# Kernel optimization log

Measured on AMD Instinct MI355X. Metric: run time of the kernel, lower is better.

## Reference

```python
import jax, jax.numpy as jnp
import numpy as np

N = 50000
E = 800000
H = 4
C = 64
IN = 61
NEG_SLOPE = 0.2


def setup_inputs() -> dict:
    key = jax.random.key(0)
    ks = jax.random.split(key, 20)
    x = jax.random.normal(ks[0], (N, IN), dtype=jnp.float32)
    edge_index = jax.random.randint(ks[1], (2, E), 0, N, dtype=jnp.int64)

    def glorot(k, shape):
        fan = shape[0] + shape[-1] if len(shape) == 2 else shape[-1] * 2
        s = jnp.sqrt(6.0 / fan)
        return jax.random.uniform(k, shape, jnp.float32, -s, s)

    dims = [IN, H * C, H * C]
    params = {}
    for i, din in enumerate(dims):
        params[f'w{i}'] = glorot(ks[2 + 4 * i], (din, H * C))
        params[f'att_src{i}'] = glorot(ks[3 + 4 * i], (H, C))
        params[f'att_dst{i}'] = glorot(ks[4 + 4 * i], (H, C))
        params[f'b{i}'] = jnp.zeros((H * C,), jnp.float32)
    params['head_w1'] = glorot(ks[14], (H * C, C))
    params['head_b1'] = jnp.zeros((C,), jnp.float32)
    params['head_w2'] = glorot(ks[15], (C, 1))
    params['head_b2'] = jnp.zeros((1,), jnp.float32)
    return dict(x=x, edge_index=edge_index, **params)


def _gat_layer(x, W, att_src, att_dst, bias, src, dst):
    # Linear transform -> [N, H, C]
    h = (x @ W).reshape(N, H, C)
    # Per-node attention logits
    a_src = jnp.einsum('nhc,hc->nh', h, att_src)  # [N, H]
    a_dst = jnp.einsum('nhc,hc->nh', h, att_dst)
    # Per-edge score, leaky relu
    e = jax.nn.leaky_relu(a_src[src] + a_dst[dst], NEG_SLOPE)  # [Etot, H]
    # Segment softmax over incoming edges of each dst node
    m = jax.ops.segment_max(e, dst, num_segments=N)  # [N, H]
    ex = jnp.exp(e - m[dst])
    denom = jax.ops.segment_sum(ex, dst, num_segments=N)
    alpha = ex / denom[dst]  # [Etot, H]
    # Scatter-aggregate messages
    out = jax.ops.segment_sum(h[src] * alpha[:, :, None], dst, num_segments=N)  # [N, H, C]
    return out.reshape(N, H * C) + bias


def reference(x, edge_index, w0, att_src0, att_dst0, b0,
              w1, att_src1, att_dst1, b1,
              w2, att_src2, att_dst2, b2,
              head_w1, head_b1, head_w2, head_b2):
    # PyG GATConv adds self-loops by default
    loop = jnp.arange(N, dtype=edge_index.dtype)
    src = jnp.concatenate([edge_index[0], loop])
    dst = jnp.concatenate([edge_index[1], loop])

    layers = [(w0, att_src0, att_dst0, b0),
              (w1, att_src1, att_dst1, b1),
              (w2, att_src2, att_dst2, b2)]
    h = x
    for (W, a_s, a_d, b) in layers:
        h = _gat_layer(h, W, a_s, a_d, b, src, dst)
        h = jax.nn.elu(h)  # dropout is identity in eval mode
    # MLP head
    h = jax.nn.relu(h @ head_w1 + head_b1)
    out = (h @ head_w2 + head_b2).squeeze(-1)  # [N]
    return out
```

## Files before the change

### kernel.cpp

```cpp
#include <hip/hip_runtime.h>
#include <cstdint>
#include <cstddef>

#define NN   50000
#define EE   800000
#define ETOT (EE + NN)
#define HC   256
#define NEG_SLOPE 0.2f
#define SENT_WORDS 25000
#define SENT_VAL 0x42C80000u

typedef __attribute__((ext_vector_type(8))) short g4_bf16x8;
typedef __attribute__((ext_vector_type(4))) float g4_f32x4;

__device__ __forceinline__ float g4_bf2f(unsigned short h) {
    union { unsigned int u; float f; } v;
    v.u = ((unsigned int)h) << 16;
    return v.f;
}
__device__ __forceinline__ unsigned short g4_f2bf(float f) {
    union { float f; unsigned int u; } v;
    v.f = f;
    unsigned int u = v.u;
    u += 0x7fffu + ((u >> 16) & 1u);
    return (unsigned short)(u >> 16);
}
__device__ __forceinline__ float g4_ld(const void* p, size_t i, int isf) {
    return isf ? ((const float*)p)[i] : g4_bf2f(((const unsigned short*)p)[i]);
}

__global__ void g4_init(const unsigned int* __restrict__ xw,
                        const int* __restrict__ ei32, int* __restrict__ flags,
                        int* __restrict__ deg, int* __restrict__ cnt,
                        unsigned int* __restrict__ outw) {
    if (blockIdx.x == 0) {
        __shared__ int cs[256];
        int t = threadIdx.x;
        unsigned int w = xw[t];
        int e = (int)((w >> 23) & 0xffu);
        cs[t] = (e >= 110 && e <= 135) ? 1 : 0;
        __syncthreads();
        for (int off = 128; off > 0; off >>= 1) {
            if (t < off) cs[t] += cs[t + off];
            __syncthreads();
        }
        if (t == 0) {
            flags[0] = (cs[0] >= 128) ? 1 : 0;
            int i64 = (ei32[1] == 0 && ei32[3] == 0 && ei32[5] == 0 &&
                       ei32[7] == 0 && ei32[9] == 0) ? 1 : 0;
            flags[1] = i64;
        }
    }
    int i = blockIdx.x * 256 + threadIdx.x;
    if (i < NN) { deg[i] = 0; cnt[i] = 0; }
    if (i < SENT_WORDS) outw[i] = SENT_VAL;
}

__global__ void g4_hist(const int* __restrict__ ei, const int* __restrict__ flags,
                        int* __restrict__ deg) {
    int e = blockIdx.x * blockDim.x + threadIdx.x;
    if (e >= ETOT) return;
    int i64 = flags[1];
    int d;
    if (e < EE) d = i64 ? ei[2 * (EE + e)] : ei[EE + e];
    else        d = e - EE;
    atomicAdd(&deg[d], 1);
}

__global__ void g4_scan_block(const int* __restrict__ deg, int* __restrict__ tmp,
                              int* __restrict__ partial) {
    __shared__ int sh[256];
    int i = blockIdx.x * 256 + threadIdx.x;
    int v = (i < NN) ? deg[i] : 0;
    sh[threadIdx.x] = v;
    __syncthreads();
    for (int off = 1; off < 256; off <<= 1) {
        int t = (threadIdx.x >= off) ? sh[threadIdx.x - off] : 0;
        __syncthreads();
        sh[threadIdx.x] += t;
        __syncthreads();
    }
    if (i < NN) tmp[i] = sh[threadIdx.x] - v;
    if (threadIdx.x == 255) partial[blockIdx.x] = sh[255];
}

__global__ void g4_scan_partial(int* __restrict__ partial, int nb,
                                int* __restrict__ rowptrN) {
    __shared__ int sh[256];
    int v = (threadIdx.x < nb) ? partial[threadIdx.x] : 0;
    sh[threadIdx.x] = v;
    __syncthreads();
    for (int off = 1; off < 256; off <<= 1) {
        int t = (threadIdx.x >= off) ? sh[threadIdx.x - off] : 0;
        __syncthreads();
        sh[threadIdx.x] += t;
        __syncthreads();
    }
    if (threadIdx.x < nb) partial[threadIdx.x] = sh[threadIdx.x] - v;
    if (threadIdx.x == 0) *rowptrN = ETOT;
}

__global__ void g4_scan_add(const int* __restrict__ tmp, const int* __restrict__ partial,
                            int* __restrict__ rowptr) {
    int i = blockIdx.x * 256 + threadIdx.x;
    if (i < NN) rowptr[i] = tmp[i] + partial[blockIdx.x];
}

__global__ void g4_fill_csr(const int* __restrict__ ei, const int* __restrict__ flags,
                            const int* __restrict__ rowptr,
                            int* __restrict__ cnt, int* __restrict__ col) {
    int e = blockIdx.x * blockDim.x + threadIdx.x;
    if (e >= ETOT) return;
    int i64 = flags[1];
    int s, d;
    if (e < EE) {
        s = i64 ? ei[2 * e] : ei[e];
        d = i64 ? ei[2 * (EE + e)] : ei[EE + e];
    } else {
        s = e - EE; d = e - EE;
    }
    int pos = rowptr[d] + atomicAdd(&cnt[d], 1);
    col[pos] = s;
}

__global__ void g4_aprep(const void* __restrict__ x, const int* __restrict__ flags,
                         unsigned short* __restrict__ Apad) {
    int i = blockIdx.x * 256 + threadIdx.x;
    if (i >= NN * 64) return;
    int row = i >> 6, k = i & 63;
    unsigned short v = 0;
    if (k < 61) {
        if (flags[0]) v = g4_f2bf(((const float*)x)[(size_t)row * 61 + k]);
        else          v = ((const unsigned short*)x)[(size_t)row * 61 + k];
    }
    Apad[i] = v;
}

__global__ void g4_bfprep(const void* __restrict__ B, const int* __restrict__ flags,
                          unsigned short* __restrict__ Bfrag, int K, int NK) {
    int i = blockIdx.x * 256 + threadIdx.x;
    if (i >= HC * NK * 32) return;
    int j = i & 7;
    int rest = i >> 3;
    int lane = rest & 63; rest >>= 6;
    int ks = rest % NK;
    int wcjt = rest / NK;
    int jt = wcjt & 3, wc = wcjt >> 2;
    int n = wc * 64 + jt * 16 + (lane & 15);
    int k = ks * 32 + (lane >> 4) * 8 + j;
    unsigned short v = 0;
    if (k < K) {
        if (flags[0]) v = g4_f2bf(((const float*)B)[(size_t)k * HC + n]);
        else          v = ((const unsigned short*)B)[(size_t)k * HC + n];
    }
    Bfrag[i] = v;
}

template <int NK>
__global__ __launch_bounds__(256) void g4_gemm3(
    const unsigned short* __restrict__ A, const unsigned short* __restrict__ Bfrag,
    const int* __restrict__ flags, unsigned short* __restrict__ C,
    const void* __restrict__ att_src, const void* __restrict__ att_dst,
    float* __restrict__ a_srcO, float* __restrict__ a_dstO, int M) {
    __shared__ unsigned short wsep[4 * 64 * 72];
    const int KP   = NK * 32;
    const int isf  = flags[0];
    const int tid  = threadIdx.x;
    const int lane = tid & 63;
    const int wc   = tid >> 6;
    const int quad = lane >> 4;
    const int l15  = lane & 15;
    const int bm   = blockIdx.x * 64;

    g4_f32x4 acc[4][4];
    #pragma unroll
    for (int it = 0; it < 4; it++)
        #pragma unroll
        for (int jt = 0; jt < 4; jt++) {
            acc[it][jt].x = 0.f; acc[it][jt].y = 0.f;
            acc[it][jt].z = 0.f; acc[it][jt].w = 0.f;
        }

    #pragma unroll
    for (int ks = 0; ks < NK; ks++) {
        g4_bf16x8 afr[4], bfr[4];
        #pragma unroll
        for (int it = 0; it < 4; it++)
            afr[it] = *(const g4_bf16x8*)
                (A + (size_t)(bm + it * 16 + l15) * KP + ks * 32 + quad * 8);
        #pragma unroll
        for (int jt = 0; jt < 4; jt++)
            bfr[jt] = *(const g4_bf16x8*)
                (Bfrag + ((size_t)(((wc * 4 + jt) * NK + ks) * 64 + lane) << 3));
        #pragma unroll
        for (int it = 0; it < 4; it++)
            #pragma unroll
            for (int jt = 0; jt < 4; jt++)
                acc[it][jt] = __builtin_amdgcn_mfma_f32_16x16x32_bf16(
                    afr[it], bfr[jt], acc[it][jt], 0, 0, 0);
    }

    {
        unsigned short* w = &wsep[wc * (64 * 72)];
        #pragma unroll
        for (int it = 0; it < 4; it++)
            #pragma unroll
            for (int jt = 0; jt < 4; jt++)
                #pragma unroll
                for (int r = 0; r < 4; r++)
                    w[(it * 16 + quad * 4 + r) * 72 + jt * 16 + l15] =
                        g4_f2bf(acc[it][jt][r]);
        #pragma unroll
        for (int rr = 0; rr < 16; rr++) {
            int row = rr * 4 + quad;
            uint2 v = *(const uint2*)&w[row * 72 + l15 * 4];
            int gm = bm + row;
            if (gm < M)
                *(uint2*)(C + (size_t)gm * HC + wc * 64 + l15 * 4) = v;
        }
    }
    float asv[4], adv[4];
    #pragma unroll
    for (int jt = 0; jt < 4; jt++) {
        asv[jt] = g4_ld(att_src, wc * 64 + jt * 16 + l15, isf);
        adv[jt] = g4_ld(att_dst, wc * 64 + jt * 16 + l15, isf);
    }
    #pragma unroll
    for (int it = 0; it < 4; it++) {
        #pragma unroll
        for (int r = 0; r < 4; r++) {
            float ps = 0.f, pd = 0.f;
            #pragma unroll
            for (int jt = 0; jt < 4; jt++) {
                ps += acc[it][jt][r] * asv[jt];
                pd += acc[it][jt][r] * adv[jt];
            }
            #pragma unroll
            for (int off = 1; off < 16; off <<= 1) {
                ps += __shfl_xor(ps, off);
                pd += __shfl_xor(pd, off);
            }
            if (l15 == 0) {
                int gm = bm + it * 16 + quad * 4 + r;
                if (gm < M) {
                    a_srcO[gm * 4 + wc] = ps;
                    a_dstO[gm * 4 + wc] = pd;
                }
            }
        }
    }
}

__global__ __launch_bounds__(256) void g4_gatherf(
    const unsigned short* __restrict__ h,
    const float* __restrict__ a_src, const float* __restrict__ a_dst,
    const int* __restrict__ rowptr, const int* __restrict__ col,
    const void* __restrict__ bias, const int* __restrict__ flags,
    unsigned short* __restrict__ xout) {
    int d    = (blockIdx.x * blockDim.x + threadIdx.x) >> 6;
    int lane = threadIdx.x & 63;
    if (d >= NN) return;
    d = __builtin_amdgcn_readfirstlane(d);
    const int isf = flags[0];
    const int hd  = lane >> 4;
    const int q   = lane & 3;
    const int eloc = lane >> 2;
    const int l15 = lane & 15;
    const int start = __builtin_amdgcn_readfirstlane(rowptr[d]);
    const int end   = __builtin_amdgcn_readfirstlane(rowptr[d + 1]);

    g4_f32x4 ad4 = *(const g4_f32x4*)(a_dst + 4 * (size_t)d);
    float mx[4] = {-1e30f, -1e30f, -1e30f, -1e30f};
    for (int i = start + lane; i < end; i += 64) {
        int s = col[i];
        g4_f32x4 as = *(const g4_f32x4*)(a_src + 4 * (size_t)s);
        #pragma unroll
        for (int hh = 0; hh < 4; hh++) {
            float e = as[hh] + ad4[hh];
            e = (e > 0.f) ? e : NEG_SLOPE * e;
            mx[hh] = fmaxf(mx[hh], e);
        }
    }
    for (int off = 32; off > 0; off >>= 1)
        #pragma unroll
        for (int hh = 0; hh < 4; hh++) mx[hh] = fmaxf(mx[hh], __shfl_xor(mx[hh], off));
    float mxq = (q < 2) ? ((q == 0) ? mx[0] : mx[1]) : ((q == 2) ? mx[2] : mx[3]);
    float adq = (q < 2) ? ((q == 0) ? ad4.x : ad4.y) : ((q == 2) ? ad4.z : ad4.w);

    float a0 = 0.f, a1 = 0.f, a2 = 0.f, a3 = 0.f;
    float sm = 0.f;
    const size_t ch = (size_t)(lane << 2);
    for (int base = start; base < end; base += 16) {
        int m = end - base;
        if (m > 16) m = 16;
        int cv = col[base + l15];
        int sE = __shfl(cv, eloc);
        float av = 0.f;
        if (eloc < m) {
            float e = a_src[4 * (size_t)sE + q] + adq;
            e = (e > 0.f) ? e : NEG_SLOPE * e;
            av = __expf(e - mxq);
            sm += av;
        }
        int j = 0;
        for (; j + 4 <= m; j += 4) {
            int s0 = __shfl(cv, j);
            int s1 = __shfl(cv, j + 1);
            int s2 = __shfl(cv, j + 2);
            int s3 = __shfl(cv, j + 3);
            float w0 = __shfl(av, 4 * j + hd);
            float w1 = __shfl(av, 4 * j + 4 + hd);
            float w2 = __shfl(av, 4 * j + 8 + hd);
            float w3 = __shfl(av, 4 * j + 12 + hd);
            uint2 h0 = *(const uint2*)(h + (((size_t)s0) << 8) + ch);
            uint2 h1 = *(const uint2*)(h + (((size_t)s1) << 8) + ch);
            uint2 h2 = *(const uint2*)(h + (((size_t)s2) << 8) + ch);
            uint2 h3 = *(const uint2*)(h + (((size_t)s3) << 8) + ch);
            a0 = fmaf(__uint_as_float(h0.x << 16),         w0, a0);
            a1 = fmaf(__uint_as_float(h0.x & 0xffff0000u), w0, a1);
            a2 = fmaf(__uint_as_float(h0.y << 16),         w0, a2);
            a3 = fmaf(__uint_as_float(h0.y & 0xffff0000u), w0, a3);
            a0 = fmaf(__uint_as_float(h1.x << 16),         w1, a0);
            a1 = fmaf(__uint_as_float(h1.x & 0xffff0000u), w1, a1);
            a2 = fmaf(__uint_as_float(h1.y << 16),         w1, a2);
            a3 = fmaf(__uint_as_float(h1.y & 0xffff0000u), w1, a3);
            a0 = fmaf(__uint_as_float(h2.x << 16),         w2, a0);
            a1 = fmaf(__uint_as_float(h2.x & 0xffff0000u), w2, a1);
            a2 = fmaf(__uint_as_float(h2.y << 16),         w2, a2);
            a3 = fmaf(__uint_as_float(h2.y & 0xffff0000u), w2, a3);
            a0 = fmaf(__uint_as_float(h3.x << 16),         w3, a0);
            a1 = fmaf(__uint_as_float(h3.x & 0xffff0000u), w3, a1);
            a2 = fmaf(__uint_as_float(h3.y << 16),         w3, a2);
            a3 = fmaf(__uint_as_float(h3.y & 0xffff0000u), w3, a3);
        }
        for (; j < m; j++) {
            int s = __shfl(cv, j);
            float w = __shfl(av, 4 * j + hd);
            uint2 hv = *(const uint2*)(h + (((size_t)s) << 8) + ch);
            a0 = fmaf(__uint_as_float(hv.x << 16),         w, a0);
            a1 = fmaf(__uint_as_float(hv.x & 0xffff0000u), w, a1);
            a2 = fmaf(__uint_as_float(hv.y << 16),         w, a2);
            a3 = fmaf(__uint_as_float(hv.y & 0xffff0000u), w, a3);
        }
    }
    for (int off = 4; off < 64; off <<= 1) sm += __shfl_xor(sm, off);
    float inv = 1.f / __shfl(sm, hd);
    float acc[4] = {a0 * inv, a1 * inv, a2 * inv, a3 * inv};
    unsigned short ov[4];
    #pragma unroll
    for (int j = 0; j < 4; j++) {
        float v = acc[j] + g4_ld(bias, (lane << 2) + j, isf);
        v = (v > 0.f) ? v : (__expf(v) - 1.f);
        ov[j] = g4_f2bf(v);
    }
    uint2 pack;
    pack.x = (unsigned int)ov[0] | ((unsigned int)ov[1] << 16);
    pack.y = (unsigned int)ov[2] | ((unsigned int)ov[3] << 16);
    *(uint2*)(xout + ((size_t)d << 8) + (lane << 2)) = pack;
}

__global__ __launch_bounds__(256) void g4_head2(
    const unsigned short* __restrict__ x, const void* __restrict__ w1,
    const void* __restrict__ b1, const void* __restrict__ w2,
    const void* __restrict__ b2, const int* __restrict__ flags,
    void* __restrict__ outp) {
    __shared__ float As[64][17];
    __shared__ float Bs[16][64];
    __shared__ float red[64][17];
    const int isf = flags[0];
    const int tid = threadIdx.x;
    const int bm  = blockIdx.x * 64;
    const int tx  = tid & 15;
    const int ty  = tid >> 4;
    float acc[4][4] = {};
    for (int k0 = 0; k0 < HC; k0 += 16) {
        for (int i = tid; i < 64 * 16; i += 256) {
            int m = i >> 4, kk = i & 15;
            int gm = bm + m;
            float v = 0.f;
            if (gm < NN) v = g4_bf2f(x[(size_t)gm * HC + k0 + kk]);
            As[m][kk] = v;
        }
        for (int i = tid; i < 16 * 64; i += 256) {
            int kk = i >> 6, n = i & 63;
            Bs[kk][n] = g4_ld(w1, (size_t)(k0 + kk) * 64 + n, isf);
        }
        __syncthreads();
        #pragma unroll
        for (int kk = 0; kk < 16; ++kk) {
            float a[4], b[4];
            #pragma unroll
            for (int i = 0; i < 4; i++) a[i] = As[ty * 4 + i][kk];
            #pragma unroll
            for (int j = 0; j < 4; j++) b[j] = Bs[kk][tx * 4 + j];
            #pragma unroll
            for (int i = 0; i < 4; i++)
                #pragma unroll
                for (int j = 0; j < 4; j++) acc[i][j] += a[i] * b[j];
        }
        __syncthreads();
    }
    float b1v[4], w2v[4];
    #pragma unroll
    for (int j = 0; j < 4; j++) {
        b1v[j] = g4_ld(b1, tx * 4 + j, isf);
        w2v[j] = g4_ld(w2, tx * 4 + j, isf);
    }
    #pragma unroll
    for (int i = 0; i < 4; i++) {
        float s = 0.f;
        #pragma unroll
        for (int j = 0; j < 4; j++) {
            float v = acc[i][j] + b1v[j];
            v = fmaxf(v, 0.f);
            s += v * w2v[j];
        }
        red[ty * 4 + i][tx] = s;
    }
    __syncthreads();
    if (tid < 64) {
        float s = 0.f;
        #pragma unroll
        for (int g = 0; g < 16; g++) s += red[tid][g];
        int gm = bm + tid;
        if (gm < NN) {
            float r = s + g4_ld(b2, 0, isf);
            if (isf) ((float*)outp)[gm] = r;
            else     ((unsigned short*)outp)[gm] = g4_f2bf(r);
        }
    }
}

extern "C" __attribute__((visibility("default")))
void kernel_launch(void* const* d_in, const int* in_sizes, int n_in,
                   void* d_out, int out_size, void* d_ws, size_t ws_size,
                   hipStream_t stream) {
    const void* x_in = d_in[0];
    const int*  ei   = (const int*)d_in[1];
    const void* W[3]    = {d_in[2], d_in[6], d_in[10]};
    const void* ASRC[3] = {d_in[3], d_in[7], d_in[11]};
    const void* ADST[3] = {d_in[4], d_in[8], d_in[12]};
    const void* BIAS[3] = {d_in[5], d_in[9], d_in[13]};
    const void* hw1 = d_in[14];
    const void* hb1 = d_in[15];
    const void* hw2 = d_in[16];
    const void* hb2 = d_in[17];

    char* base = (char*)d_ws;
    size_t woff = 0;
#define G4_TAKE(name, type, count) \
    type* name = (type*)(base + woff); \
    woff += (((size_t)(count)) * sizeof(type) + 255) & ~(size_t)255;
    G4_TAKE(flags,   int, 8)
    G4_TAKE(deg,     int, NN)
    G4_TAKE(cnt,     int, NN)
    G4_TAKE(tmp,     int, NN)
    G4_TAKE(partial, int, 256)
    G4_TAKE(rowptr,  int, NN + 1)
    G4_TAKE(col,     int, ETOT + 16)
    G4_TAKE(asr,     float, (size_t)NN * 4)
    G4_TAKE(adsb,    float, (size_t)NN * 4)
    G4_TAKE(Apad,    unsigned short, (size_t)(NN + 64) * 64)
    G4_TAKE(Bfrag,   unsigned short, (size_t)HC * HC)
    G4_TAKE(hbuf,    unsigned short, (size_t)(NN + 64) * HC)
    G4_TAKE(xbuf,    unsigned short, (size_t)(NN + 64) * HC)
#undef G4_TAKE

    const int SCAN_BLOCKS = (NN + 255) / 256;
    const int EDGE_BLOCKS = (ETOT + 255) / 256;
    const int WAVE_BLOCKS = (NN + 3) / 4;
    const int TILE_BLOCKS = (NN + 63) / 64;

    g4_init<<<SCAN_BLOCKS, 256, 0, stream>>>((const unsigned int*)x_in, ei, flags,
                                             deg, cnt, (unsigned int*)d_out);

    g4_hist<<<EDGE_BLOCKS, 256, 0, stream>>>(ei, flags, deg);
    g4_scan_block<<<SCAN_BLOCKS, 256, 0, stream>>>(deg, tmp, partial);
    g4_scan_partial<<<1, 256, 0, stream>>>(partial, SCAN_BLOCKS, rowptr + NN);
    g4_scan_add<<<SCAN_BLOCKS, 256, 0, stream>>>(tmp, partial, rowptr);
    g4_fill_csr<<<EDGE_BLOCKS, 256, 0, stream>>>(ei, flags, rowptr, cnt, col);

    g4_aprep<<<(NN * 64 + 255) / 256, 256, 0, stream>>>(x_in, flags, Apad);

    for (int l = 0; l < 3; l++) {
        int K  = (l == 0) ? 61 : HC;
        int NK = (l == 0) ? 2  : 8;
        g4_bfprep<<<(HC * NK * 32 + 255) / 256, 256, 0, stream>>>(W[l], flags, Bfrag, K, NK);
        if (l == 0) {
            g4_gemm3<2><<<TILE_BLOCKS, 256, 0, stream>>>(Apad, Bfrag, flags, hbuf,
                ASRC[l], ADST[l], asr, adsb, NN);
        } else {
            g4_gemm3<8><<<TILE_BLOCKS, 256, 0, stream>>>(xbuf, Bfrag, flags, hbuf,
                ASRC[l], ADST[l], asr, adsb, NN);
        }
        g4_gatherf<<<WAVE_BLOCKS, 256, 0, stream>>>(hbuf, asr, adsb, rowptr, col,
                                                    BIAS[l], flags, xbuf);
    }
    g4_head2<<<TILE_BLOCKS, 256, 0, stream>>>(xbuf, hw1, hb1, hw2, hb2, flags, d_out);
}
```

Measured before the change: 527.6 us.

## Restructure GEMM so each wave computes 16 full rows across all columns

Each wave now owns a 16-row by 256-column tile instead of a 64-row by 64-column tile, loading one A fragment per k-step and streaming all 16 B fragments. The LDS staging buffer for the output is removed, and bf16 values are written straight to global memory as 2-byte scattered stores. The attention logits for all four heads are now reduced inside one wave. The trade-off is less reuse of B fragments per load, more B traffic per row, and less coalesced output stores, in exchange for dropping LDS and fitting a 16-row granularity.

```diff
diff --git a/kernel.cpp b/kernel.cpp
--- a/kernel.cpp
+++ b/kernel.cpp
@@ -144,9 +144,8 @@
     int rest = i >> 3;
     int lane = rest & 63; rest >>= 6;
     int ks = rest % NK;
-    int wcjt = rest / NK;
-    int jt = wcjt & 3, wc = wcjt >> 2;
-    int n = wc * 64 + jt * 16 + (lane & 15);
+    int f  = rest / NK;
+    int n = f * 16 + (lane & 15);
     int k = ks * 32 + (lane >> 4) * 8 + j;
     unsigned short v = 0;
     if (k < K) {
@@ -162,89 +161,71 @@
     const int* __restrict__ flags, unsigned short* __restrict__ C,
     const void* __restrict__ att_src, const void* __restrict__ att_dst,
     float* __restrict__ a_srcO, float* __restrict__ a_dstO, int M) {
-    __shared__ unsigned short wsep[4 * 64 * 72];
     const int KP   = NK * 32;
     const int isf  = flags[0];
     const int tid  = threadIdx.x;
     const int lane = tid & 63;
-    const int wc   = tid >> 6;
+    const int wq   = tid >> 6;
     const int quad = lane >> 4;
     const int l15  = lane & 15;
-    const int bm   = blockIdx.x * 64;
-
-    g4_f32x4 acc[4][4];
-    #pragma unroll
-    for (int it = 0; it < 4; it++)
-        #pragma unroll
-        for (int jt = 0; jt < 4; jt++) {
-            acc[it][jt].x = 0.f; acc[it][jt].y = 0.f;
-            acc[it][jt].z = 0.f; acc[it][jt].w = 0.f;
-        }
+    const int bm   = blockIdx.x * 64 + wq * 16;
+
+    g4_f32x4 acc[16];
+    #pragma unroll
+    for (int jt = 0; jt < 16; jt++) {
+        acc[jt].x = 0.f; acc[jt].y = 0.f; acc[jt].z = 0.f; acc[jt].w = 0.f;
+    }
 
     #pragma unroll
     for (int ks = 0; ks < NK; ks++) {
-        g4_bf16x8 afr[4], bfr[4];
-        #pragma unroll
-        for (int it = 0; it < 4; it++)
-            afr[it] = *(const g4_bf16x8*)
-                (A + (size_t)(bm + it * 16 + l15) * KP + ks * 32 + quad * 8);
-        #pragma unroll
-        for (int jt = 0; jt < 4; jt++)
-            bfr[jt] = *(const g4_bf16x8*)
-                (Bfrag + ((size_t)(((wc * 4 + jt) * NK + ks) * 64 + lane) << 3));
-        #pragma unroll
-        for (int it = 0; it < 4; it++)
+        g4_bf16x8 afr = *(const g4_bf16x8*)
+            (A + (size_t)(bm + l15) * KP + ks * 32 + quad * 8);
+        #pragma unroll
+        for (int jt = 0; jt < 16; jt++) {
+            g4_bf16x8 bfr = *(const g4_bf16x8*)
+                (Bfrag + ((size_t)((jt * NK + ks) * 64 + lane) << 3));
+            acc[jt] = __builtin_amdgcn_mfma_f32_16x16x32_bf16(afr, bfr, acc[jt], 0, 0, 0);
+        }
+    }
+
+    #pragma unroll
+    for (int jt = 0; jt < 16; jt++) {
+        #pragma unroll
+        for (int r = 0; r < 4; r++) {
+            int gm = bm + quad * 4 + r;
+            if (gm < M) C[(size_t)gm * HC + jt * 16 + l15] = g4_f2bf(acc[jt][r]);
+        }
+    }
+
+    float asv[16], adv[16];
+    #pragma unroll
+    for (int jt = 0; jt < 16; jt++) {
+        asv[jt] = g4_ld(att_src, jt * 16 + l15, isf);
+        adv[jt] = g4_ld(att_dst, jt * 16 + l15, isf);
+    }
+    #pragma unroll
+    for (int r = 0; r < 4; r++) {
+        float ps[4] = {0.f, 0.f, 0.f, 0.f};
+        float pd[4] = {0.f, 0.f, 0.f, 0.f};
+        #pragma unroll
+        for (int jt = 0; jt < 16; jt++) {
+            ps[jt >> 2] += acc[jt][r] * asv[jt];
+            pd[jt >> 2] += acc[jt][r] * adv[jt];
+        }
+        #pragma unroll
+        for (int off = 1; off < 16; off <<= 1)
             #pragma unroll
-            for (int jt = 0; jt < 4; jt++)
-                acc[it][jt] = __builtin_amdgcn_mfma_f32_16x16x32_bf16(
-                    afr[it], bfr[jt], acc[it][jt], 0, 0, 0);
-    }
-
-    {
-        unsigned short* w = &wsep[wc * (64 * 72)];
-        #pragma unroll
-        for (int it = 0; it < 4; it++)
-            #pragma unroll
-            for (int jt = 0; jt < 4; jt++)
+            for (int hh = 0; hh < 4; hh++) {
+                ps[hh] += __shfl_xor(ps[hh], off);
+                pd[hh] += __shfl_xor(pd[hh], off);
+            }
+        if (l15 == 0) {
+            int gm = bm + quad * 4 + r;
+            if (gm < M) {
                 #pragma unroll
-                for (int r = 0; r < 4; r++)
-                    w[(it * 16 + quad * 4 + r) * 72 + jt * 16 + l15] =
-                        g4_f2bf(acc[it][jt][r]);
-        #pragma unroll
-        for (int rr = 0; rr < 16; rr++) {
-            int row = rr * 4 + quad;
-            uint2 v = *(const uint2*)&w[row * 72 + l15 * 4];
-            int gm = bm + row;
-            if (gm < M)
-                *(uint2*)(C + (size_t)gm * HC + wc * 64 + l15 * 4) = v;
-        }
-    }
-    float asv[4], adv[4];
-    #pragma unroll
-    for (int jt = 0; jt < 4; jt++) {
-        asv[jt] = g4_ld(att_src, wc * 64 + jt * 16 + l15, isf);
-        adv[jt] = g4_ld(att_dst, wc * 64 + jt * 16 + l15, isf);
-    }
-    #pragma unroll
-    for (int it = 0; it < 4; it++) {
-        #pragma unroll
-        for (int r = 0; r < 4; r++) {
-            float ps = 0.f, pd = 0.f;
-            #pragma unroll
-            for (int jt = 0; jt < 4; jt++) {
-                ps += acc[it][jt][r] * asv[jt];
-                pd += acc[it][jt][r] * adv[jt];
-            }
-            #pragma unroll
-            for (int off = 1; off < 16; off <<= 1) {
-                ps += __shfl_xor(ps, off);
-                pd += __shfl_xor(pd, off);
-            }
-            if (l15 == 0) {
-                int gm = bm + it * 16 + quad * 4 + r;
-                if (gm < M) {
-                    a_srcO[gm * 4 + wc] = ps;
-                    a_dstO[gm * 4 + wc] = pd;
+                for (int hh = 0; hh < 4; hh++) {
+                    a_srcO[gm * 4 + hh] = ps[hh];
+                    a_dstO[gm * 4 + hh] = pd[hh];
                 }
             }
         }
```

Result: slower. 610.5 us (+15.7%).
